# Optimization experiments

Hardware: AMD Instinct MI355X
Metric: run time of the kernel (lower is better)

## Reference

```python
import jax, jax.numpy as jnp
import numpy as np

B, C, H, W = 16, 512, 32, 32
MID = max(8, C // 4)      # gate hidden
CA_MID = max(8, C // 4)   # channel-attn hidden
LOW_RADIUS = 0.35


def dct_mat(N):
    # Orthonormal DCT-II matrix: D[k,n] = s_k * sqrt(2/N) * cos(pi*(2n+1)*k/(2N))
    k = jnp.arange(N, dtype=jnp.float32)[:, None]
    n = jnp.arange(N, dtype=jnp.float32)[None, :]
    M = jnp.cos(jnp.pi * (2.0 * n + 1.0) * k / (2.0 * N)) * jnp.sqrt(2.0 / N)
    return M.at[0].multiply(1.0 / jnp.sqrt(2.0))


def build_low_mask(Hh, Ww, low_radius):
    yy = jnp.arange(Hh, dtype=jnp.float32)[:, None] / max(Hh - 1, 1)
    xx = jnp.arange(Ww, dtype=jnp.float32)[None, :] / max(Ww - 1, 1)
    rr = jnp.sqrt(yy ** 2 + xx ** 2)
    rr = rr / jnp.maximum(rr.max(), 1e-6)
    return (rr <= low_radius).astype(jnp.float32)[None, None]  # [1,1,H,W]


def conv1x1(x, w, b):
    # x: [B,Cin,H,W], w: [Cout,Cin], b: [Cout]
    return jnp.einsum('bchw,oc->bohw', x, w) + b[None, :, None, None]


def freq_transform(x, gw1, gb1, gw2, gb2, Dh, Dw, lm):
    # gate: avgpool -> 1x1 -> relu -> 1x1 -> sigmoid, output 2 scalars per sample
    pooled = jnp.mean(x, axis=(2, 3), keepdims=True)  # [B,C,1,1]
    g = jax.nn.sigmoid(conv1x1(jax.nn.relu(conv1x1(pooled, gw1, gb1)), gw2, gb2))
    g_low, g_high = g[:, 0:1], g[:, 1:2]  # [B,1,1,1]
    # 2D ortho DCT: Dh @ x @ Dw^T
    freq = jnp.einsum('ih,bchw->bciw', Dh, x)
    freq = jnp.einsum('jw,bchw->bchj', Dw, freq)
    # frequency gating fused
    gated = freq * (g_low * lm + g_high * (1.0 - lm))
    # inverse: Dh^T @ freq @ Dw
    out = jnp.einsum('hi,bchw->bciw', Dh, gated)
    out = jnp.einsum('wj,bchw->bchj', Dw, out)
    return out


def setup_inputs() -> dict:
    key = jax.random.key(0)
    ks = jax.random.split(key, 24)
    s = 1.0 / np.sqrt(C)
    d = {
        'rgb': jax.random.normal(ks[0], (B, C, H, W), jnp.float32),
        'dsm': jax.random.normal(ks[1], (B, C, H, W), jnp.float32),
        'rgb_w': jax.random.normal(ks[2], (C, C), jnp.float32) * s,
        'rgb_b': jax.random.normal(ks[3], (C,), jnp.float32) * 0.01,
        'dsm_w': jax.random.normal(ks[4], (C, C), jnp.float32) * s,
        'dsm_b': jax.random.normal(ks[5], (C,), jnp.float32) * 0.01,
        'gate_w1': jax.random.normal(ks[6], (MID, C), jnp.float32) * s,
        'gate_b1': jax.random.normal(ks[7], (MID,), jnp.float32) * 0.01,
        'gate_w2': jax.random.normal(ks[8], (2, MID), jnp.float32) * (1.0 / np.sqrt(MID)),
        'gate_b2': jax.random.normal(ks[9], (2,), jnp.float32) * 0.01,
        'q_w': jax.random.normal(ks[10], (C, C), jnp.float32) * s,
        'q_b': jax.random.normal(ks[11], (C,), jnp.float32) * 0.01,
        'k_w': jax.random.normal(ks[12], (C, C), jnp.float32) * s,
        'k_b': jax.random.normal(ks[13], (C,), jnp.float32) * 0.01,
        'v_w': jax.random.normal(ks[14], (C, C), jnp.float32) * s,
        'v_b': jax.random.normal(ks[15], (C,), jnp.float32) * 0.01,
        'sp_w': jax.random.normal(ks[16], (C, C, 3, 3), jnp.float32) * (s / 3.0),
        'sp_b': jax.random.normal(ks[17], (C,), jnp.float32) * 0.01,
        'ca_w1': jax.random.normal(ks[18], (CA_MID, C), jnp.float32) * s,
        'ca_b1': jax.random.normal(ks[19], (CA_MID,), jnp.float32) * 0.01,
        'ca_w2': jax.random.normal(ks[20], (C, CA_MID), jnp.float32) * (1.0 / np.sqrt(CA_MID)),
        'ca_b2': jax.random.normal(ks[21], (C,), jnp.float32) * 0.01,
    }
    return d


def reference(rgb, dsm, rgb_w, rgb_b, dsm_w, dsm_b, gate_w1, gate_b1, gate_w2, gate_b2,
              q_w, q_b, k_w, k_b, v_w, v_b, sp_w, sp_b, ca_w1, ca_b1, ca_w2, ca_b2):
    Dh, Dw = dct_mat(H), dct_mat(W)
    lm = build_low_mask(H, W, LOW_RADIUS)

    rgb_p = conv1x1(rgb, rgb_w, rgb_b)
    dsm_p = conv1x1(dsm, dsm_w, dsm_b)

    rgb_f = freq_transform(rgb_p, gate_w1, gate_b1, gate_w2, gate_b2, Dh, Dw, lm)
    dsm_f = freq_transform(dsm_p, gate_w1, gate_b1, gate_w2, gate_b2, Dh, Dw, lm)

    q = conv1x1(rgb_f, q_w, q_b).reshape(B, C, H * W)
    k = conv1x1(dsm_f, k_w, k_b).reshape(B, C, H * W)
    v = conv1x1(dsm_f, v_w, v_b).reshape(B, C, H * W)

    # attn over spatial tokens: [B,N,N]
    scores = jnp.einsum('bcn,bcm->bnm', q, k) / jnp.sqrt(jnp.float32(C))
    attn = jax.nn.softmax(scores, axis=-1)
    out = jnp.einsum('bnm,bcm->bcn', attn, v).reshape(B, C, H, W)

    spatial = jax.lax.conv_general_dilated(
        out, sp_w, window_strides=(1, 1), padding='SAME',
        dimension_numbers=('NCHW', 'OIHW', 'NCHW')) + sp_b[None, :, None, None]

    pooled = jnp.mean(spatial, axis=(2, 3), keepdims=True)
    weight = jax.nn.sigmoid(conv1x1(jax.nn.relu(conv1x1(pooled, ca_w1, ca_b1)), ca_w2, ca_b2))
    return rgb_p + spatial * weight
```

## Files before the change

### kernel.cpp

```cpp
#include <hip/hip_runtime.h>

typedef long long i64;
typedef unsigned int u32;
typedef unsigned short u16;

#define Bq 16
#define Cq 512
#define Hq 32
#define Wq 32
#define Nq 1024
#define MIDq 128
#define XPBq 591872

typedef __attribute__((ext_vector_type(8))) short bf16x8;
typedef __attribute__((ext_vector_type(4))) float f32x4;

static __device__ __forceinline__ u16 f2bf(float f) {
  u32 u = __float_as_uint(f);
  u = (u + 0x7FFFu + ((u >> 16) & 1u)) >> 16;
  return (u16)u;
}
static __device__ __forceinline__ float bf2f(u16 h) {
  return __uint_as_float(((u32)h) << 16);
}

__global__ void k_dct_mask(float* __restrict__ D, float* __restrict__ lm) {
  int t = threadIdx.x;
  int i = t >> 5, j = t & 31;
  float v = cosf(3.14159265358979323846f * (2.0f * j + 1.0f) * (float)i / 64.0f) * 0.25f;
  if (i == 0) v *= 0.7071067811865476f;
  D[t] = v;
  float yy = i * (1.0f / 31.0f), xx = j * (1.0f / 31.0f);
  float rr = sqrtf(yy * yy + xx * xx) * 0.7071067811865476f;
  lm[t] = (rr <= 0.35f) ? 1.0f : 0.0f;
}

__global__ __launch_bounds__(256) void k_split(
    const float* __restrict__ src, u16* __restrict__ hi, u16* __restrict__ lo) {
  i64 idx = ((i64)blockIdx.x * 256 + threadIdx.x) * 4;
  float4 f = *(const float4*)(src + idx);
  ushort4 h, l;
  h.x = f2bf(f.x); l.x = f2bf(f.x - bf2f(h.x));
  h.y = f2bf(f.y); l.y = f2bf(f.y - bf2f(h.y));
  h.z = f2bf(f.z); l.z = f2bf(f.z - bf2f(h.z));
  h.w = f2bf(f.w); l.w = f2bf(f.w - bf2f(h.w));
  *(ushort4*)(hi + idx) = h;
  *(ushort4*)(lo + idx) = l;
}

__global__ __launch_bounds__(256) void k_zero(u16* __restrict__ p) {
  i64 idx = ((i64)blockIdx.x * 256 + threadIdx.x) * 8;
  *(uint4*)(p + idx) = (uint4){0u, 0u, 0u, 0u};
}

__global__ __launch_bounds__(256) void k_wsplit9(
    const float* __restrict__ w, u16* __restrict__ h9, u16* __restrict__ l9) {
  int idx = blockIdx.x * 256 + threadIdx.x;
  int o = idx >> 7;
  int c4 = (idx & 127) << 2;
  float vals[4][9];
#pragma unroll
  for (int j = 0; j < 4; j++) {
    const float* wp = w + ((i64)o * Cq + c4 + j) * 9;
#pragma unroll
    for (int t = 0; t < 9; t++) vals[j][t] = wp[t];
  }
#pragma unroll
  for (int t = 0; t < 9; t++) {
    ushort4 h, l;
    h.x = f2bf(vals[0][t]); l.x = f2bf(vals[0][t] - bf2f(h.x));
    h.y = f2bf(vals[1][t]); l.y = f2bf(vals[1][t] - bf2f(h.y));
    h.z = f2bf(vals[2][t]); l.z = f2bf(vals[2][t] - bf2f(h.z));
    h.w = f2bf(vals[3][t]); l.w = f2bf(vals[3][t] - bf2f(h.w));
    i64 od = (i64)t * (Cq * Cq) + (i64)o * Cq + c4;
    *(ushort4*)(h9 + od) = h;
    *(ushort4*)(l9 + od) = l;
  }
}

__global__ __launch_bounds__(256) void k_split_t(
    const float* __restrict__ src, u16* __restrict__ hi, u16* __restrict__ lo) {
  __shared__ float ld[64][65];
  int b = blockIdx.z;
  int c0 = blockIdx.y << 6;
  int n0 = blockIdx.x << 6;
  int tid = threadIdx.x;
  const float* s = src + (i64)b * (Cq * Nq);
  u16* ph = hi + (i64)b * (Cq * Nq);
  u16* pl = lo + (i64)b * (Cq * Nq);
#pragma unroll
  for (int p = 0; p < 4; p++) {
    int row = (tid >> 4) + p * 16;
    int col4 = (tid & 15) << 2;
    *(float4*)&ld[row][col4] = *(const float4*)(s + (i64)(c0 + row) * Nq + n0 + col4);
  }
  __syncthreads();
#pragma unroll
  for (int p = 0; p < 4; p++) {
    int nr = (tid >> 4) + p * 16;
    int c4 = (tid & 15) << 2;
    float f0 = ld[c4 + 0][nr], f1 = ld[c4 + 1][nr];
    float f2 = ld[c4 + 2][nr], f3 = ld[c4 + 3][nr];
    ushort4 h, l;
    h.x = f2bf(f0); l.x = f2bf(f0 - bf2f(h.x));
    h.y = f2bf(f1); l.y = f2bf(f1 - bf2f(h.y));
    h.z = f2bf(f2); l.z = f2bf(f2 - bf2f(h.z));
    h.w = f2bf(f3); l.w = f2bf(f3 - bf2f(h.w));
    i64 o = (i64)(n0 + nr) * Cq + c0 + c4;
    *(ushort4*)(ph + o) = h;
    *(ushort4*)(pl + o) = l;
  }
}

__global__ __launch_bounds__(256) void k_padsplit_t(
    const float* __restrict__ src, u16* __restrict__ hi, u16* __restrict__ lo) {
  __shared__ float ld[64][65];
  int b = blockIdx.z;
  int c0 = blockIdx.y << 6;
  int n0 = blockIdx.x << 6;
  int tid = threadIdx.x;
  const float* s = src + (i64)b * (Cq * Nq);
  u16* ph = hi + (i64)b * XPBq;
  u16* pl = lo + (i64)b * XPBq;
#pragma unroll
  for (int p = 0; p < 4; p++) {
    int row = (tid >> 4) + p * 16;
    int col4 = (tid & 15) << 2;
    *(float4*)&ld[row][col4] = *(const float4*)(s + (i64)(c0 + row) * Nq + n0 + col4);
  }
  __syncthreads();
#pragma unroll
  for (int p = 0; p < 4; p++) {
    int nr = (tid >> 4) + p * 16;
    int c4 = (tid & 15) << 2;
    float f0 = ld[c4 + 0][nr], f1 = ld[c4 + 1][nr];
    float f2 = ld[c4 + 2][nr], f3 = ld[c4 + 3][nr];
    ushort4 h, l;
    h.x = f2bf(f0); l.x = f2bf(f0 - bf2f(h.x));
    h.y = f2bf(f1); l.y = f2bf(f1 - bf2f(h.y));
    h.z = f2bf(f2); l.z = f2bf(f2 - bf2f(h.z));
    h.w = f2bf(f3); l.w = f2bf(f3 - bf2f(h.w));
    int n = n0 + nr;
    int pr = ((n >> 5) + 1) * 34 + (n & 31) + 1;
    i64 o = (i64)pr * Cq + c0 + c4;
    *(ushort4*)(ph + o) = h;
    *(ushort4*)(pl + o) = l;
  }
}

__global__ __launch_bounds__(256) void k_gemm(
    const u16* __restrict__ Ahi, const u16* __restrict__ Alo, i64 sAb,
    const u16* __restrict__ Bhi, const u16* __restrict__ Blo, i64 sBb,
    const float* __restrict__ bias, int bias_mode, float scale,
    int M, int N, int K,
    float* __restrict__ Cf, u16* __restrict__ Chi, u16* __restrict__ Clo,
    i64 sCb, int out_mode) {
  __shared__ __align__(16) u16 As_h[128][40];
  __shared__ __align__(16) u16 As_l[128][40];
  __shared__ __align__(16) u16 Bs_h[128][40];
  __shared__ __align__(16) u16 Bs_l[128][40];
  int tid = threadIdx.x;
  int b = blockIdx.z;
  int m0 = blockIdx.y << 7;
  int n0 = blockIdx.x << 7;
  const u16* pAhi = Ahi + (i64)b * sAb;
  const u16* pAlo = Alo + (i64)b * sAb;
  const u16* pBhi = Bhi + (i64)b * sBb;
  const u16* pBlo = Blo + (i64)b * sBb;
  int lane = tid & 63;
  int wid = tid >> 6;
  int wm = (wid & 1) << 6;
  int wn = (wid >> 1) << 6;
  int l15 = lane & 15;
  int g8 = (lane >> 4) << 3;
  f32x4 acc[4][4];
#pragma unroll
  for (int mi = 0; mi < 4; mi++)
#pragma unroll
    for (int nj = 0; nj < 4; nj++)
      acc[mi][nj] = (f32x4){0.f, 0.f, 0.f, 0.f};

  for (int k0 = 0; k0 < K; k0 += 32) {
#pragma unroll
    for (int i = 0; i < 8; i++) {
      const int arr = i >> 1;
      const int r = ((i & 1) << 6) + (tid >> 2);
      const int seg = tid & 3;
      uint4 val;
      if (arr == 0)      val = *(const uint4*)(pAhi + (i64)(m0 + r) * K + k0 + seg * 8);
      else if (arr == 1) val = *(const uint4*)(pAlo + (i64)(m0 + r) * K + k0 + seg * 8);
      else if (arr == 2) val = *(const uint4*)(pBhi + (i64)(n0 + r) * K + k0 + seg * 8);
      else               val = *(const uint4*)(pBlo + (i64)(n0 + r) * K + k0 + seg * 8);
      if (arr == 0)      *(uint4*)&As_h[r][seg * 8] = val;
      else if (arr == 1) *(uint4*)&As_l[r][seg * 8] = val;
      else if (arr == 2) *(uint4*)&Bs_h[r][seg * 8] = val;
      else               *(uint4*)&Bs_l[r][seg * 8] = val;
    }
    __syncthreads();
    bf16x8 ah[4], al[4], bh[4], bl[4];
#pragma unroll
    for (int mi = 0; mi < 4; mi++) {
      int row = wm + mi * 16 + l15;
      ah[mi] = *(const bf16x8*)&As_h[row][g8];
      al[mi] = *(const bf16x8*)&As_l[row][g8];
    }
#pragma unroll
    for (int nj = 0; nj < 4; nj++) {
      int row = wn + nj * 16 + l15;
      bh[nj] = *(const bf16x8*)&Bs_h[row][g8];
      bl[nj] = *(const bf16x8*)&Bs_l[row][g8];
    }
#pragma unroll
    for (int mi = 0; mi < 4; mi++)
#pragma unroll
      for (int nj = 0; nj < 4; nj++) {
        acc[mi][nj] = __builtin_amdgcn_mfma_f32_16x16x32_bf16(ah[mi], bh[nj], acc[mi][nj], 0, 0, 0);
        acc[mi][nj] = __builtin_amdgcn_mfma_f32_16x16x32_bf16(ah[mi], bl[nj], acc[mi][nj], 0, 0, 0);
        acc[mi][nj] = __builtin_amdgcn_mfma_f32_16x16x32_bf16(al[mi], bh[nj], acc[mi][nj], 0, 0, 0);
      }
    __syncthreads();
  }

#pragma unroll
  for (int mi = 0; mi < 4; mi++)
#pragma unroll
    for (int nj = 0; nj < 4; nj++) {
      int col_g = n0 + wn + nj * 16 + l15;
#pragma unroll
      for (int r = 0; r < 4; r++) {
        int row_g = m0 + wm + mi * 16 + ((lane >> 4) << 2) + r;
        float val = acc[mi][nj][r] * scale;
        if (bias_mode == 1) val += bias[row_g];
        else if (bias_mode == 2) val += bias[col_g];
        i64 o = (i64)b * sCb + (i64)row_g * N + col_g;
        if (out_mode == 0) {
          Cf[o] = val;
        } else {
          u16 h = f2bf(val);
          Chi[o] = h;
          Clo[o] = f2bf(val - bf2f(h));
        }
      }
    }
}

__global__ __launch_bounds__(256) void k_conv3_mfma(
    const u16* __restrict__ Wh, const u16* __restrict__ Wl,
    const u16* __restrict__ Xh, const u16* __restrict__ Xl,
    const float* __restrict__ bias, float* __restrict__ out) {
  __shared__ __align__(16) u16 As_h[128][40];
  __shared__ __align__(16) u16 As_l[128][40];
  __shared__ __align__(16) u16 Bs_h[128][40];
  __shared__ __align__(16) u16 Bs_l[128][40];
  int tid = threadIdx.x;
  int b = blockIdx.z;
  int m0 = blockIdx.y << 7;
  int n0 = blockIdx.x << 7;
  const u16* pXh = Xh + (i64)b * XPBq;
  const u16* pXl = Xl + (i64)b * XPBq;
  int lane = tid & 63;
  int wid = tid >> 6;
  int wm = (wid & 1) << 6;
  int wn = (wid >> 1) << 6;
  int l15 = lane & 15;
  int g8 = (lane >> 4) << 3;
  int rr = tid >> 2, seg = tid & 3;
  int n_a = n0 + rr, n_b = n0 + 64 + rr;
  int prb0 = (n_a >> 5) * 34 + (n_a & 31);
  int prb1 = (n_b >> 5) * 34 + (n_b & 31);
  f32x4 acc[4][4];
#pragma unroll
  for (int mi = 0; mi < 4; mi++)
#pragma unroll
    for (int nj = 0; nj < 4; nj++)
      acc[mi][nj] = (f32x4){0.f, 0.f, 0.f, 0.f};

  for (int tap = 0; tap < 9; tap++) {
    int doff = (tap / 3) * 34 + (tap % 3);
    const u16* wth = Wh + (i64)tap * (Cq * Cq);
    const u16* wtl = Wl + (i64)tap * (Cq * Cq);
    i64 bb0 = (i64)(prb0 + doff) * Cq + seg * 8;
    i64 bb1 = (i64)(prb1 + doff) * Cq + seg * 8;
    for (int c0 = 0; c0 < Cq; c0 += 32) {
      *(uint4*)&As_h[rr][seg * 8]      = *(const uint4*)(wth + (i64)(m0 + rr) * Cq + c0 + seg * 8);
      *(uint4*)&As_h[64 + rr][seg * 8] = *(const uint4*)(wth + (i64)(m0 + 64 + rr) * Cq + c0 + seg * 8);
      *(uint4*)&As_l[rr][seg * 8]      = *(const uint4*)(wtl + (i64)(m0 + rr) * Cq + c0 + seg * 8);
      *(uint4*)&As_l[64 + rr][seg * 8] = *(const uint4*)(wtl + (i64)(m0 + 64 + rr) * Cq + c0 + seg * 8);
      *(uint4*)&Bs_h[rr][seg * 8]      = *(const uint4*)(pXh + bb0 + c0);
      *(uint4*)&Bs_h[64 + rr][seg * 8] = *(const uint4*)(pXh + bb1 + c0);
      *(uint4*)&Bs_l[rr][seg * 8]      = *(const uint4*)(pXl + bb0 + c0);
      *(uint4*)&Bs_l[64 + rr][seg * 8] = *(const uint4*)(pXl + bb1 + c0);
      __syncthreads();
      bf16x8 ah[4], al[4], bh[4], bl[4];
#pragma unroll
      for (int mi = 0; mi < 4; mi++) {
        int row = wm + mi * 16 + l15;
        ah[mi] = *(const bf16x8*)&As_h[row][g8];
        al[mi] = *(const bf16x8*)&As_l[row][g8];
      }
#pragma unroll
      for (int nj = 0; nj < 4; nj++) {
        int row = wn + nj * 16 + l15;
        bh[nj] = *(const bf16x8*)&Bs_h[row][g8];
        bl[nj] = *(const bf16x8*)&Bs_l[row][g8];
      }
#pragma unroll
      for (int mi = 0; mi < 4; mi++)
#pragma unroll
        for (int nj = 0; nj < 4; nj++) {
          acc[mi][nj] = __builtin_amdgcn_mfma_f32_16x16x32_bf16(ah[mi], bh[nj], acc[mi][nj], 0, 0, 0);
          acc[mi][nj] = __builtin_amdgcn_mfma_f32_16x16x32_bf16(ah[mi], bl[nj], acc[mi][nj], 0, 0, 0);
          acc[mi][nj] = __builtin_amdgcn_mfma_f32_16x16x32_bf16(al[mi], bh[nj], acc[mi][nj], 0, 0, 0);
        }
      __syncthreads();
    }
  }

#pragma unroll
  for (int mi = 0; mi < 4; mi++)
#pragma unroll
    for (int nj = 0; nj < 4; nj++) {
      int col_g = n0 + wn + nj * 16 + l15;
#pragma unroll
      for (int r = 0; r < 4; r++) {
        int row_g = m0 + wm + mi * 16 + ((lane >> 4) << 2) + r;
        float val = acc[mi][nj][r] + bias[row_g];
        out[(i64)b * (Cq * Nq) + (i64)row_g * Nq + col_g] = val;
      }
    }
}

__global__ __launch_bounds__(256) void k_pool(const float* __restrict__ x, float* __restrict__ o) {
  int gw = (int)((blockIdx.x * 256 + threadIdx.x) >> 6);
  int ln = threadIdx.x & 63;
  const float* p = x + (i64)gw * Nq;
  float s = 0.f;
#pragma unroll
  for (int it = 0; it < 4; it++) {
    float4 v = *(const float4*)(p + ln * 4 + it * 256);
    s += v.x + v.y + v.z + v.w;
  }
#pragma unroll
  for (int off = 32; off > 0; off >>= 1) s += __shfl_xor(s, off, 64);
  if (ln == 0) o[gw] = s * (1.0f / 1024.0f);
}

__global__ __launch_bounds__(128) void k_gate(
    const float* __restrict__ pooled, const float* __restrict__ w1,
    const float* __restrict__ b1, const float* __restrict__ w2,
    const float* __restrict__ b2, float* __restrict__ g) {
  __shared__ float pl[Cq];
  __shared__ float h[MIDq];
  int b = blockIdx.x, tid = threadIdx.x;
  for (int c = tid; c < Cq; c += 128) pl[c] = pooled[b * Cq + c];
  __syncthreads();
  float s = b1[tid];
  const float* wr = w1 + (i64)tid * Cq;
  for (int c = 0; c < Cq; c++) s = fmaf(wr[c], pl[c], s);
  h[tid] = fmaxf(s, 0.f);
  __syncthreads();
  if (tid < 2) {
    float t = b2[tid];
    const float* w2r = w2 + tid * MIDq;
    for (int m = 0; m < MIDq; m++) t = fmaf(w2r[m], h[m], t);
    g[b * 2 + tid] = 1.0f / (1.0f + expf(-t));
  }
}

__global__ __launch_bounds__(256) void k_freq(
    const float* __restrict__ xr, const float* __restrict__ xd,
    float* __restrict__ yr, float* __restrict__ yd,
    const float* __restrict__ g_r, const float* __restrict__ g_d,
    const float* __restrict__ Dm, const float* __restrict__ lm) {
  __shared__ float Ds[32][36], Dt[32][36], Xs[32][36], T1[32][36];
  int bid = blockIdx.x;
  const float* x; float* y; const float* g;
  if (bid < Bq * Cq) {
    x = xr + (i64)bid * Nq; y = yr + (i64)bid * Nq; g = g_r + (bid >> 9) * 2;
  } else {
    int id = bid - Bq * Cq;
    x = xd + (i64)id * Nq; y = yd + (i64)id * Nq; g = g_d + (id >> 9) * 2;
  }
  int tid = threadIdx.x;
  int r_ = tid >> 3, j4 = (tid & 7) << 2;
  {
    float4 dv = *(const float4*)(Dm + tid * 4);
    *(float4*)&Ds[r_][j4] = dv;
    Dt[j4 + 0][r_] = dv.x; Dt[j4 + 1][r_] = dv.y;
    Dt[j4 + 2][r_] = dv.z; Dt[j4 + 3][r_] = dv.w;
    *(float4*)&Xs[r_][j4] = *(const float4*)(x + tid * 4);
  }
  float gl = g[0], gh = g[1];
  __syncthreads();
  float a0 = 0, a1 = 0, a2 = 0, a3 = 0;
#pragma unroll
  for (int h = 0; h < 32; h++) {
    float a = Ds[r_][h];
    float4 bv = *(const float4*)&Xs[h][j4];
    a0 = fmaf(a, bv.x, a0); a1 = fmaf(a, bv.y, a1);
    a2 = fmaf(a, bv.z, a2); a3 = fmaf(a, bv.w, a3);
  }
  *(float4*)&T1[r_][j4] = make_float4(a0, a1, a2, a3);
  __syncthreads();
  a0 = a1 = a2 = a3 = 0;
#pragma unroll
  for (int w = 0; w < 32; w++) {
    float a = T1[r_][w];
    float4 bv = *(const float4*)&Dt[w][j4];
    a0 = fmaf(a, bv.x, a0); a1 = fmaf(a, bv.y, a1);
    a2 = fmaf(a, bv.z, a2); a3 = fmaf(a, bv.w, a3);
  }
  {
    float4 mv = *(const float4*)(lm + r_ * 32 + j4);
    a0 *= fmaf(gl, mv.x, gh * (1.f - mv.x));
    a1 *= fmaf(gl, mv.y, gh * (1.f - mv.y));
    a2 *= fmaf(gl, mv.z, gh * (1.f - mv.z));
    a3 *= fmaf(gl, mv.w, gh * (1.f - mv.w));
  }
  __syncthreads();
  *(float4*)&Xs[r_][j4] = make_float4(a0, a1, a2, a3);
  __syncthreads();
  a0 = a1 = a2 = a3 = 0;
#pragma unroll
  for (int ii = 0; ii < 32; ii++) {
    float a = Dt[r_][ii];
    float4 bv = *(const float4*)&Xs[ii][j4];
    a0 = fmaf(a, bv.x, a0); a1 = fmaf(a, bv.y, a1);
    a2 = fmaf(a, bv.z, a2); a3 = fmaf(a, bv.w, a3);
  }
  __syncthreads();
  *(float4*)&T1[r_][j4] = make_float4(a0, a1, a2, a3);
  __syncthreads();
  a0 = a1 = a2 = a3 = 0;
#pragma unroll
  for (int jj = 0; jj < 32; jj++) {
    float a = T1[r_][jj];
    float4 bv = *(const float4*)&Ds[jj][j4];
    a0 = fmaf(a, bv.x, a0); a1 = fmaf(a, bv.y, a1);
    a2 = fmaf(a, bv.z, a2); a3 = fmaf(a, bv.w, a3);
  }
  *(float4*)(y + tid * 4) = make_float4(a0, a1, a2, a3);
}

__global__ __launch_bounds__(256) void k_softmax_split(
    const float* __restrict__ sc, u16* __restrict__ ahi, u16* __restrict__ alo) {
  __shared__ float redm[4], reds[4];
  i64 row = blockIdx.x;
  const float* p = sc + row * (i64)Nq;
  int tid = threadIdx.x;
  float4 v = ((const float4*)p)[tid];
  float mx = fmaxf(fmaxf(v.x, v.y), fmaxf(v.z, v.w));
#pragma unroll
  for (int o = 32; o > 0; o >>= 1) mx = fmaxf(mx, __shfl_xor(mx, o, 64));
  if ((tid & 63) == 0) redm[tid >> 6] = mx;
  __syncthreads();
  mx = fmaxf(fmaxf(redm[0], redm[1]), fmaxf(redm[2], redm[3]));
  v.x = expf(v.x - mx); v.y = expf(v.y - mx);
  v.z = expf(v.z - mx); v.w = expf(v.w - mx);
  float s = v.x + v.y + v.z + v.w;
#pragma unroll
  for (int o = 32; o > 0; o >>= 1) s += __shfl_xor(s, o, 64);
  if ((tid & 63) == 0) reds[tid >> 6] = s;
  __syncthreads();
  s = reds[0] + reds[1] + reds[2] + reds[3];
  float inv = 1.0f / s;
  v.x *= inv; v.y *= inv; v.z *= inv; v.w *= inv;
  ushort4 h, l;
  h.x = f2bf(v.x); l.x = f2bf(v.x - bf2f(h.x));
  h.y = f2bf(v.y); l.y = f2bf(v.y - bf2f(h.y));
  h.z = f2bf(v.z); l.z = f2bf(v.z - bf2f(h.z));
  h.w = f2bf(v.w); l.w = f2bf(v.w - bf2f(h.w));
  *(ushort4*)(ahi + row * Nq + tid * 4) = h;
  *(ushort4*)(alo + row * Nq + tid * 4) = l;
}

__global__ __launch_bounds__(512) void k_ca(
    const float* __restrict__ pooled, const float* __restrict__ w1,
    const float* __restrict__ b1, const float* __restrict__ w2,
    const float* __restrict__ b2, float* __restrict__ wt) {
  __shared__ float pl[Cq];
  __shared__ float h[MIDq];
  int b = blockIdx.x, tid = threadIdx.x;
  pl[tid] = pooled[b * Cq + tid];
  __syncthreads();
  if (tid < MIDq) {
    float s = b1[tid];
    const float* wr = w1 + (i64)tid * Cq;
    for (int c = 0; c < Cq; c++) s = fmaf(wr[c], pl[c], s);
    h[tid] = fmaxf(s, 0.f);
  }
  __syncthreads();
  float s = b2[tid];
  const float* wr = w2 + (i64)tid * MIDq;
  for (int m = 0; m < MIDq; m++) s = fmaf(wr[m], h[m], s);
  wt[b * Cq + tid] = 1.0f / (1.0f + expf(-s));
}

__global__ __launch_bounds__(256) void k_final(
    const float* __restrict__ rgbp, const float* __restrict__ sp,
    const float* __restrict__ wt, float* __restrict__ out) {
  i64 idx = (i64)blockIdx.x * 256 + threadIdx.x;
  float4 a = ((const float4*)rgbp)[idx];
  float4 s = ((const float4*)sp)[idx];
  float w = wt[idx >> 8];
  float4 r;
  r.x = fmaf(s.x, w, a.x); r.y = fmaf(s.y, w, a.y);
  r.z = fmaf(s.z, w, a.z); r.w = fmaf(s.w, w, a.w);
  ((float4*)out)[idx] = r;
}

extern "C" void kernel_launch(void* const* d_in, const int* in_sizes, int n_in,
                              void* d_out, int out_size, void* d_ws, size_t ws_size,
                              hipStream_t stream) {
  (void)in_sizes; (void)n_in; (void)out_size; (void)ws_size;
  const float* rgb    = (const float*)d_in[0];
  const float* dsm    = (const float*)d_in[1];
  const float* rgb_w  = (const float*)d_in[2];
  const float* rgb_b  = (const float*)d_in[3];
  const float* dsm_w  = (const float*)d_in[4];
  const float* dsm_b  = (const float*)d_in[5];
  const float* gate_w1 = (const float*)d_in[6];
  const float* gate_b1 = (const float*)d_in[7];
  const float* gate_w2 = (const float*)d_in[8];
  const float* gate_b2 = (const float*)d_in[9];
  const float* q_w = (const float*)d_in[10];
  const float* q_b = (const float*)d_in[11];
  const float* k_w = (const float*)d_in[12];
  const float* k_b = (const float*)d_in[13];
  const float* v_w = (const float*)d_in[14];
  const float* v_b = (const float*)d_in[15];
  const float* sp_w = (const float*)d_in[16];
  const float* sp_b = (const float*)d_in[17];
  const float* ca_w1 = (const float*)d_in[18];
  const float* ca_b1 = (const float*)d_in[19];
  const float* ca_w2 = (const float*)d_in[20];
  const float* ca_b2 = (const float*)d_in[21];

  const i64 S  = (i64)Bq * Cq * Nq;
  const i64 SU = S;
  const i64 WE = (i64)Cq * Cq;
  const i64 XPT = (i64)Bq * XPBq;

  float* wsf = (float*)d_ws;
  float* rgbp   = wsf;
  float* dsmp   = wsf + S;
  float* rgbf   = wsf + 2 * S;
  float* dsmf   = wsf + 3 * S;
  float* scores  = dsmp;
  float* attout  = dsmf;
  float* spatial = dsmp;
  float* smallr = wsf + 4 * S;
  float* Dm     = smallr;
  float* lm     = smallr + 1024;
  float* pooled = smallr + 2048;
  float* g_rgb  = smallr + 10240;
  float* g_dsm  = smallr + 10272;
  float* wt     = smallr + 10304;
  u16* ub = (u16*)(wsf + 4 * S + 32768);
  u16* U0 = ub;          u16* U1 = ub + SU;
  u16* U2 = ub + 2 * SU; u16* U3 = ub + 3 * SU;
  u16* U4 = ub + 4 * SU; u16* U5 = ub + 5 * SU;
  u16* XPh = ub;
  u16* XPl = ub + XPT;
  u16* wb = ub + 6 * SU;
  u16* rgbw_h = wb;           u16* rgbw_l = wb + WE;
  u16* dsmw_h = wb + 2 * WE;  u16* dsmw_l = wb + 3 * WE;
  u16* qw_h   = wb + 4 * WE;  u16* qw_l   = wb + 5 * WE;
  u16* kw_h   = wb + 6 * WE;  u16* kw_l   = wb + 7 * WE;
  u16* vw_h   = wb + 8 * WE;  u16* vw_l   = wb + 9 * WE;
  u16* w9h    = wb + 10 * WE; u16* w9l    = wb + 19 * WE;

  const i64 sT = (i64)Nq * Cq;
  const i64 sS = (i64)Nq * Nq;
  const float rsqc = 0.044194173824159216f;

  k_dct_mask<<<1, 1024, 0, stream>>>(Dm, lm);

  k_split<<<WE / 1024, 256, 0, stream>>>(rgb_w, rgbw_h, rgbw_l);
  k_split<<<WE / 1024, 256, 0, stream>>>(dsm_w, dsmw_h, dsmw_l);
  k_split<<<WE / 1024, 256, 0, stream>>>(q_w, qw_h, qw_l);
  k_split<<<WE / 1024, 256, 0, stream>>>(k_w, kw_h, kw_l);
  k_split<<<WE / 1024, 256, 0, stream>>>(v_w, vw_h, vw_l);
  k_wsplit9<<<256, 256, 0, stream>>>(sp_w, w9h, w9l);

  dim3 gT(Nq / 64, Cq / 64, Bq);
  dim3 gW(Nq / 128, Cq / 128, Bq);
  dim3 gQ(Cq / 128, Nq / 128, Bq);
  dim3 gS(Nq / 128, Nq / 128, Bq);

  k_split_t<<<gT, 256, 0, stream>>>(rgb, U0, U1);
  k_gemm<<<gW, 256, 0, stream>>>(rgbw_h, rgbw_l, 0, U0, U1, sT,
                                 rgb_b, 1, 1.0f, Cq, Nq, Cq,
                                 rgbp, nullptr, nullptr, sT, 0);
  k_split_t<<<gT, 256, 0, stream>>>(dsm, U0, U1);
  k_gemm<<<gW, 256, 0, stream>>>(dsmw_h, dsmw_l, 0, U0, U1, sT,
                                 dsm_b, 1, 1.0f, Cq, Nq, Cq,
                                 dsmp, nullptr, nullptr, sT, 0);

  k_pool<<<(Bq * Cq) / 4, 256, 0, stream>>>(rgbp, pooled);
  k_gate<<<Bq, 128, 0, stream>>>(pooled, gate_w1, gate_b1, gate_w2, gate_b2, g_rgb);
  k_pool<<<(Bq * Cq) / 4, 256, 0, stream>>>(dsmp, pooled);
  k_gate<<<Bq, 128, 0, stream>>>(pooled, gate_w1, gate_b1, gate_w2, gate_b2, g_dsm);

  k_freq<<<2 * Bq * Cq, 256, 0, stream>>>(rgbp, dsmp, rgbf, dsmf, g_rgb, g_dsm, Dm, lm);

  k_split_t<<<gT, 256, 0, stream>>>(rgbf, U0, U1);
  k_split_t<<<gT, 256, 0, stream>>>(dsmf, U2, U3);

  k_gemm<<<gQ, 256, 0, stream>>>(U0, U1, sT, qw_h, qw_l, 0,
                                 q_b, 2, 1.0f, Nq, Cq, Cq,
                                 nullptr, U4, U5, sT, 1);
  k_gemm<<<gQ, 256, 0, stream>>>(U2, U3, sT, kw_h, kw_l, 0,
                                 k_b, 2, 1.0f, Nq, Cq, Cq,
                                 nullptr, U0, U1, sT, 1);
  k_gemm<<<gS, 256, 0, stream>>>(U4, U5, sT, U0, U1, sT,
                                 nullptr, 0, rsqc, Nq, Nq, Cq,
                                 scores, nullptr, nullptr, sS, 0);
  k_gemm<<<gW, 256, 0, stream>>>(vw_h, vw_l, 0, U2, U3, sT,
                                 v_b, 1, 1.0f, Cq, Nq, Cq,
                                 nullptr, U4, U5, sT, 1);
  k_softmax_split<<<Bq * Nq, 256, 0, stream>>>(scores, U0, U2);
  k_gemm<<<gW, 256, 0, stream>>>(U4, U5, sT, U0, U2, sS,
                                 nullptr, 0, 1.0f, Cq, Nq, Nq,
                                 attout, nullptr, nullptr, sT, 0);

  k_zero<<<(int)(2 * XPT / 8 / 256), 256, 0, stream>>>(XPh);
  k_padsplit_t<<<gT, 256, 0, stream>>>(attout, XPh, XPl);
  k_conv3_mfma<<<dim3(Nq / 128, Cq / 128, Bq), 256, 0, stream>>>(
      w9h, w9l, XPh, XPl, sp_b, spatial);

  k_pool<<<(Bq * Cq) / 4, 256, 0, stream>>>(spatial, pooled);
  k_ca<<<Bq, 512, 0, stream>>>(pooled, ca_w1, ca_b1, ca_w2, ca_b2, wt);

  k_final<<<(int)(S / 4 / 256), 256, 0, stream>>>(rgbp, spatial, wt, (float*)d_out);
}
```

Measured before the change: 857.1 us.

## Fuse fp32 split into GEMM loads, merge prep kernels, remap workgroups across XCDs

The GEMM can now read fp32 activations directly and split them into bf16 hi/lo inside the shared-memory load, so the separate transpose-and-split passes over rgb, dsm, rgbf and dsmf go away. All weight splitting and the DCT/mask setup are merged into one prep kernel. Pool and gate run as single launches over both branches. Only the padding border is zeroed instead of the whole padded buffer. GEMM and conv workgroup indices are remapped round-robin over 8 chunks to spread them across XCDs. The in-GEMM split adds conversion ALU work and strided fp32 loads to every K tile, and the low half is now truncated rather than rounded.

```diff
diff --git a/kernel.cpp b/kernel.cpp
--- a/kernel.cpp
+++ b/kernel.cpp
@@ -24,92 +24,79 @@
   return __uint_as_float(((u32)h) << 16);
 }
 
-__global__ void k_dct_mask(float* __restrict__ D, float* __restrict__ lm) {
-  int t = threadIdx.x;
-  int i = t >> 5, j = t & 31;
-  float v = cosf(3.14159265358979323846f * (2.0f * j + 1.0f) * (float)i / 64.0f) * 0.25f;
-  if (i == 0) v *= 0.7071067811865476f;
-  D[t] = v;
-  float yy = i * (1.0f / 31.0f), xx = j * (1.0f / 31.0f);
-  float rr = sqrtf(yy * yy + xx * xx) * 0.7071067811865476f;
-  lm[t] = (rr <= 0.35f) ? 1.0f : 0.0f;
-}
-
-__global__ __launch_bounds__(256) void k_split(
-    const float* __restrict__ src, u16* __restrict__ hi, u16* __restrict__ lo) {
-  i64 idx = ((i64)blockIdx.x * 256 + threadIdx.x) * 4;
-  float4 f = *(const float4*)(src + idx);
-  ushort4 h, l;
-  h.x = f2bf(f.x); l.x = f2bf(f.x - bf2f(h.x));
-  h.y = f2bf(f.y); l.y = f2bf(f.y - bf2f(h.y));
-  h.z = f2bf(f.z); l.z = f2bf(f.z - bf2f(h.z));
-  h.w = f2bf(f.w); l.w = f2bf(f.w - bf2f(h.w));
-  *(ushort4*)(hi + idx) = h;
-  *(ushort4*)(lo + idx) = l;
-}
-
-__global__ __launch_bounds__(256) void k_zero(u16* __restrict__ p) {
-  i64 idx = ((i64)blockIdx.x * 256 + threadIdx.x) * 8;
-  *(uint4*)(p + idx) = (uint4){0u, 0u, 0u, 0u};
-}
-
-__global__ __launch_bounds__(256) void k_wsplit9(
-    const float* __restrict__ w, u16* __restrict__ h9, u16* __restrict__ l9) {
-  int idx = blockIdx.x * 256 + threadIdx.x;
-  int o = idx >> 7;
-  int c4 = (idx & 127) << 2;
-  float vals[4][9];
-#pragma unroll
-  for (int j = 0; j < 4; j++) {
-    const float* wp = w + ((i64)o * Cq + c4 + j) * 9;
-#pragma unroll
-    for (int t = 0; t < 9; t++) vals[j][t] = wp[t];
-  }
-#pragma unroll
-  for (int t = 0; t < 9; t++) {
+__global__ __launch_bounds__(256) void k_prep(
+    const float* __restrict__ rgb_w, const float* __restrict__ dsm_w,
+    const float* __restrict__ q_w, const float* __restrict__ k_w,
+    const float* __restrict__ v_w, const float* __restrict__ sp_w,
+    u16* __restrict__ rw_h, u16* __restrict__ rw_l,
+    u16* __restrict__ dw_h, u16* __restrict__ dw_l,
+    u16* __restrict__ qw_h, u16* __restrict__ qw_l,
+    u16* __restrict__ kw_h, u16* __restrict__ kw_l,
+    u16* __restrict__ vw_h, u16* __restrict__ vw_l,
+    u16* __restrict__ w9h, u16* __restrict__ w9l,
+    float* __restrict__ Dm, float* __restrict__ lm) {
+  int blk = blockIdx.x, tid = threadIdx.x;
+  if (blk < 1280) {
+    int wi = blk >> 8;
+    const float* src = wi == 0 ? rgb_w : wi == 1 ? dsm_w : wi == 2 ? q_w : wi == 3 ? k_w : v_w;
+    u16* hi = wi == 0 ? rw_h : wi == 1 ? dw_h : wi == 2 ? qw_h : wi == 3 ? kw_h : vw_h;
+    u16* lo = wi == 0 ? rw_l : wi == 1 ? dw_l : wi == 2 ? qw_l : wi == 3 ? kw_l : vw_l;
+    i64 idx = ((i64)(blk & 255) * 256 + tid) * 4;
+    float4 f = *(const float4*)(src + idx);
     ushort4 h, l;
-    h.x = f2bf(vals[0][t]); l.x = f2bf(vals[0][t] - bf2f(h.x));
-    h.y = f2bf(vals[1][t]); l.y = f2bf(vals[1][t] - bf2f(h.y));
-    h.z = f2bf(vals[2][t]); l.z = f2bf(vals[2][t] - bf2f(h.z));
-    h.w = f2bf(vals[3][t]); l.w = f2bf(vals[3][t] - bf2f(h.w));
-    i64 od = (i64)t * (Cq * Cq) + (i64)o * Cq + c4;
-    *(ushort4*)(h9 + od) = h;
-    *(ushort4*)(l9 + od) = l;
-  }
-}
-
-__global__ __launch_bounds__(256) void k_split_t(
-    const float* __restrict__ src, u16* __restrict__ hi, u16* __restrict__ lo) {
-  __shared__ float ld[64][65];
-  int b = blockIdx.z;
-  int c0 = blockIdx.y << 6;
-  int n0 = blockIdx.x << 6;
-  int tid = threadIdx.x;
-  const float* s = src + (i64)b * (Cq * Nq);
-  u16* ph = hi + (i64)b * (Cq * Nq);
-  u16* pl = lo + (i64)b * (Cq * Nq);
-#pragma unroll
-  for (int p = 0; p < 4; p++) {
-    int row = (tid >> 4) + p * 16;
-    int col4 = (tid & 15) << 2;
-    *(float4*)&ld[row][col4] = *(const float4*)(s + (i64)(c0 + row) * Nq + n0 + col4);
-  }
-  __syncthreads();
-#pragma unroll
-  for (int p = 0; p < 4; p++) {
-    int nr = (tid >> 4) + p * 16;
-    int c4 = (tid & 15) << 2;
-    float f0 = ld[c4 + 0][nr], f1 = ld[c4 + 1][nr];
-    float f2 = ld[c4 + 2][nr], f3 = ld[c4 + 3][nr];
-    ushort4 h, l;
-    h.x = f2bf(f0); l.x = f2bf(f0 - bf2f(h.x));
-    h.y = f2bf(f1); l.y = f2bf(f1 - bf2f(h.y));
-    h.z = f2bf(f2); l.z = f2bf(f2 - bf2f(h.z));
-    h.w = f2bf(f3); l.w = f2bf(f3 - bf2f(h.w));
-    i64 o = (i64)(n0 + nr) * Cq + c0 + c4;
-    *(ushort4*)(ph + o) = h;
-    *(ushort4*)(pl + o) = l;
-  }
+    h.x = f2bf(f.x); l.x = f2bf(f.x - bf2f(h.x));
+    h.y = f2bf(f.y); l.y = f2bf(f.y - bf2f(h.y));
+    h.z = f2bf(f.z); l.z = f2bf(f.z - bf2f(h.z));
+    h.w = f2bf(f.w); l.w = f2bf(f.w - bf2f(h.w));
+    *(ushort4*)(hi + idx) = h;
+    *(ushort4*)(lo + idx) = l;
+  } else if (blk < 1536) {
+    int idx = (blk - 1280) * 256 + tid;
+    int o = idx >> 7;
+    int c4 = (idx & 127) << 2;
+    float vals[4][9];
+#pragma unroll
+    for (int j = 0; j < 4; j++) {
+      const float* wp = sp_w + ((i64)o * Cq + c4 + j) * 9;
+#pragma unroll
+      for (int t = 0; t < 9; t++) vals[j][t] = wp[t];
+    }
+#pragma unroll
+    for (int t = 0; t < 9; t++) {
+      ushort4 h, l;
+      h.x = f2bf(vals[0][t]); l.x = f2bf(vals[0][t] - bf2f(h.x));
+      h.y = f2bf(vals[1][t]); l.y = f2bf(vals[1][t] - bf2f(h.y));
+      h.z = f2bf(vals[2][t]); l.z = f2bf(vals[2][t] - bf2f(h.z));
+      h.w = f2bf(vals[3][t]); l.w = f2bf(vals[3][t] - bf2f(h.w));
+      i64 od = (i64)t * (Cq * Cq) + (i64)o * Cq + c4;
+      *(ushort4*)(w9h + od) = h;
+      *(ushort4*)(w9l + od) = l;
+    }
+  } else {
+#pragma unroll
+    for (int q4 = 0; q4 < 4; q4++) {
+      int t = tid * 4 + q4;
+      int i = t >> 5, j = t & 31;
+      float v = cosf(3.14159265358979323846f * (2.0f * j + 1.0f) * (float)i / 64.0f) * 0.25f;
+      if (i == 0) v *= 0.7071067811865476f;
+      Dm[t] = v;
+      float yy = i * (1.0f / 31.0f), xx = j * (1.0f / 31.0f);
+      float rr = sqrtf(yy * yy + xx * xx) * 0.7071067811865476f;
+      lm[t] = (rr <= 0.35f) ? 1.0f : 0.0f;
+    }
+  }
+}
+
+__global__ __launch_bounds__(64) void k_zero_border(u16* __restrict__ xp) {
+  int i = blockIdx.x;
+  int b = blockIdx.y;
+  int arr = blockIdx.z;
+  int pr;
+  if (i < 34) pr = i;
+  else if (i < 68) pr = 33 * 34 + (i - 34);
+  else { int j = i - 68; pr = (1 + (j >> 1)) * 34 + (j & 1) * 33; }
+  u16* p = xp + (i64)arr * ((i64)Bq * XPBq) + (i64)b * XPBq + (i64)pr * Cq;
+  *(uint4*)(p + threadIdx.x * 8) = (uint4){0u, 0u, 0u, 0u};
 }
 
 __global__ __launch_bounds__(256) void k_padsplit_t(
@@ -149,8 +136,10 @@
 }
 
 __global__ __launch_bounds__(256) void k_gemm(
-    const u16* __restrict__ Ahi, const u16* __restrict__ Alo, i64 sAb,
-    const u16* __restrict__ Bhi, const u16* __restrict__ Blo, i64 sBb,
+    const u16* __restrict__ Ahi, const u16* __restrict__ Alo,
+    const float* __restrict__ Af32, int a_mode, i64 sAb,
+    const u16* __restrict__ Bhi, const u16* __restrict__ Blo,
+    const float* __restrict__ Bf32, int b_mode, i64 sBb,
     const float* __restrict__ bias, int bias_mode, float scale,
     int M, int N, int K,
     float* __restrict__ Cf, u16* __restrict__ Chi, u16* __restrict__ Clo,
@@ -160,13 +149,20 @@
   __shared__ __align__(16) u16 Bs_h[128][40];
   __shared__ __align__(16) u16 Bs_l[128][40];
   int tid = threadIdx.x;
-  int b = blockIdx.z;
-  int m0 = blockIdx.y << 7;
-  int n0 = blockIdx.x << 7;
-  const u16* pAhi = Ahi + (i64)b * sAb;
-  const u16* pAlo = Alo + (i64)b * sAb;
-  const u16* pBhi = Bhi + (i64)b * sBb;
-  const u16* pBlo = Blo + (i64)b * sBb;
+  int gx = gridDim.x, gxy = gx * gridDim.y;
+  int nwg = gxy * gridDim.z;
+  int orig = blockIdx.x + gx * blockIdx.y + gxy * blockIdx.z;
+  int wg = (nwg & 7) ? orig : ((orig & 7) * (nwg >> 3) + (orig >> 3));
+  int b = wg / gxy;
+  int rem = wg - b * gxy;
+  int m0 = (rem / gx) << 7;
+  int n0 = (rem - (rem / gx) * gx) << 7;
+  const u16* pAhi = Ahi + (i64)b * (a_mode ? 0 : sAb);
+  const u16* pAlo = Alo + (i64)b * (a_mode ? 0 : sAb);
+  const float* pAf = a_mode ? (Af32 + (i64)b * sAb) : nullptr;
+  const u16* pBhi = Bhi + (i64)b * (b_mode ? 0 : sBb);
+  const u16* pBlo = Blo + (i64)b * (b_mode ? 0 : sBb);
+  const float* pBf = b_mode ? (Bf32 + (i64)b * sBb) : nullptr;
   int lane = tid & 63;
   int wid = tid >> 6;
   int wm = (wid & 1) << 6;
@@ -181,20 +177,65 @@
       acc[mi][nj] = (f32x4){0.f, 0.f, 0.f, 0.f};
 
   for (int k0 = 0; k0 < K; k0 += 32) {
-#pragma unroll
-    for (int i = 0; i < 8; i++) {
-      const int arr = i >> 1;
-      const int r = ((i & 1) << 6) + (tid >> 2);
-      const int seg = tid & 3;
-      uint4 val;
-      if (arr == 0)      val = *(const uint4*)(pAhi + (i64)(m0 + r) * K + k0 + seg * 8);
-      else if (arr == 1) val = *(const uint4*)(pAlo + (i64)(m0 + r) * K + k0 + seg * 8);
-      else if (arr == 2) val = *(const uint4*)(pBhi + (i64)(n0 + r) * K + k0 + seg * 8);
-      else               val = *(const uint4*)(pBlo + (i64)(n0 + r) * K + k0 + seg * 8);
-      if (arr == 0)      *(uint4*)&As_h[r][seg * 8] = val;
-      else if (arr == 1) *(uint4*)&As_l[r][seg * 8] = val;
-      else if (arr == 2) *(uint4*)&Bs_h[r][seg * 8] = val;
-      else               *(uint4*)&Bs_l[r][seg * 8] = val;
+    if (a_mode == 0) {
+#pragma unroll
+      for (int i = 0; i < 4; i++) {
+        int r = ((i & 1) << 6) + (tid >> 2);
+        int seg = tid & 3;
+        const u16* src = (i < 2) ? pAhi : pAlo;
+        uint4 val = *(const uint4*)(src + (i64)(m0 + r) * K + k0 + seg * 8);
+        if (i < 2) *(uint4*)&As_h[r][seg * 8] = val;
+        else       *(uint4*)&As_l[r][seg * 8] = val;
+      }
+    } else {
+      int cs = tid >> 6, ns = tid & 63;
+      const float* src = pAf + (i64)(k0 + cs * 8) * M + m0 + ns * 2;
+      float2 f[8];
+#pragma unroll
+      for (int j = 0; j < 8; j++) f[j] = *(const float2*)(src + (i64)j * M);
+#pragma unroll
+      for (int i = 0; i < 2; i++) {
+        union { u16 u[8]; uint4 v; } hh, ll;
+#pragma unroll
+        for (int j = 0; j < 8; j++) {
+          float x = i ? f[j].y : f[j].x;
+          u16 h = f2bf(x);
+          hh.u[j] = h;
+          ll.u[j] = (u16)(__float_as_uint(x - bf2f(h)) >> 16);
+        }
+        *(uint4*)&As_h[2 * ns + i][8 * cs] = hh.v;
+        *(uint4*)&As_l[2 * ns + i][8 * cs] = ll.v;
+      }
+    }
+    if (b_mode == 0) {
+#pragma unroll
+      for (int i = 0; i < 4; i++) {
+        int r = ((i & 1) << 6) + (tid >> 2);
+        int seg = tid & 3;
+        const u16* src = (i < 2) ? pBhi : pBlo;
+        uint4 val = *(const uint4*)(src + (i64)(n0 + r) * K + k0 + seg * 8);
+        if (i < 2) *(uint4*)&Bs_h[r][seg * 8] = val;
+        else       *(uint4*)&Bs_l[r][seg * 8] = val;
+      }
+    } else {
+      int cs = tid >> 6, ns = tid & 63;
+      const float* src = pBf + (i64)(k0 + cs * 8) * N + n0 + ns * 2;
+      float2 f[8];
+#pragma unroll
+      for (int j = 0; j < 8; j++) f[j] = *(const float2*)(src + (i64)j * N);
+#pragma unroll
+      for (int i = 0; i < 2; i++) {
+        union { u16 u[8]; uint4 v; } hh, ll;
+#pragma unroll
+        for (int j = 0; j < 8; j++) {
+          float x = i ? f[j].y : f[j].x;
+          u16 h = f2bf(x);
+          hh.u[j] = h;
+          ll.u[j] = (u16)(__float_as_uint(x - bf2f(h)) >> 16);
+        }
+        *(uint4*)&Bs_h[2 * ns + i][8 * cs] = hh.v;
+        *(uint4*)&Bs_l[2 * ns + i][8 * cs] = ll.v;
+      }
     }
     __syncthreads();
     bf16x8 ah[4], al[4], bh[4], bl[4];
@@ -253,9 +294,14 @@
   __shared__ __align__(16) u16 Bs_h[128][40];
   __shared__ __align__(16) u16 Bs_l[128][40];
   int tid = threadIdx.x;
-  int b = blockIdx.z;
-  int m0 = blockIdx.y << 7;
-  int n0 = blockIdx.x << 7;
+  int gx = gridDim.x, gxy = gx * gridDim.y;
+  int nwg = gxy * gridDim.z;
+  int orig = blockIdx.x + gx * blockIdx.y + gxy * blockIdx.z;
+  int wg = (nwg & 7) ? orig : ((orig & 7) * (nwg >> 3) + (orig >> 3));
+  int b = wg / gxy;
+  int rem = wg - b * gxy;
+  int m0 = (rem / gx) << 7;
+  int n0 = (rem - (rem / gx) * gx) << 7;
   const u16* pXh = Xh + (i64)b * XPBq;
   const u16* pXl = Xl + (i64)b * XPBq;
   int lane = tid & 63;
@@ -351,8 +397,8 @@
     const float* __restrict__ b2, float* __restrict__ g) {
   __shared__ float pl[Cq];
   __shared__ float h[MIDq];
-  int b = blockIdx.x, tid = threadIdx.x;
-  for (int c = tid; c < Cq; c += 128) pl[c] = pooled[b * Cq + c];
+  int bb = blockIdx.x, tid = threadIdx.x;
+  for (int c = tid; c < Cq; c += 128) pl[c] = pooled[bb * Cq + c];
   __syncthreads();
   float s = b1[tid];
   const float* wr = w1 + (i64)tid * Cq;
@@ -363,7 +409,7 @@
     float t = b2[tid];
     const float* w2r = w2 + tid * MIDq;
     for (int m = 0; m < MIDq; m++) t = fmaf(w2r[m], h[m], t);
-    g[b * 2 + tid] = 1.0f / (1.0f + expf(-t));
+    g[bb * 2 + tid] = 1.0f / (1.0f + expf(-t));
   }
 }
 
@@ -553,13 +599,13 @@
   float* Dm     = smallr;
   float* lm     = smallr + 1024;
   float* pooled = smallr + 2048;
-  float* g_rgb  = smallr + 10240;
-  float* g_dsm  = smallr + 10272;
-  float* wt     = smallr + 10304;
+  float* g_all  = smallr + 18432;
+  float* wt     = smallr + 18496;
   u16* ub = (u16*)(wsf + 4 * S + 32768);
   u16* U0 = ub;          u16* U1 = ub + SU;
   u16* U2 = ub + 2 * SU; u16* U3 = ub + 3 * SU;
   u16* U4 = ub + 4 * SU; u16* U5 = ub + 5 * SU;
+  (void)U1; (void)U3; (void)U5;
   u16* XPh = ub;
   u16* XPl = ub + XPT;
   u16* wb = ub + 6 * SU;
@@ -574,58 +620,52 @@
   const i64 sS = (i64)Nq * Nq;
   const float rsqc = 0.044194173824159216f;
 
-  k_dct_mask<<<1, 1024, 0, stream>>>(Dm, lm);
-
-  k_split<<<WE / 1024, 256, 0, stream>>>(rgb_w, rgbw_h, rgbw_l);
-  k_split<<<WE / 1024, 256, 0, stream>>>(dsm_w, dsmw_h, dsmw_l);
-  k_split<<<WE / 1024, 256, 0, stream>>>(q_w, qw_h, qw_l);
-  k_split<<<WE / 1024, 256, 0, stream>>>(k_w, kw_h, kw_l);
-  k_split<<<WE / 1024, 256, 0, stream>>>(v_w, vw_h, vw_l);
-  k_wsplit9<<<256, 256, 0, stream>>>(sp_w, w9h, w9l);
-
-  dim3 gT(Nq / 64, Cq / 64, Bq);
+  k_prep<<<1537, 256, 0, stream>>>(rgb_w, dsm_w, q_w, k_w, v_w, sp_w,
+                                   rgbw_h, rgbw_l, dsmw_h, dsmw_l, qw_h, qw_l,
+                                   kw_h, kw_l, vw_h, vw_l, w9h, w9l, Dm, lm);
+
   dim3 gW(Nq / 128, Cq / 128, Bq);
   dim3 gQ(Cq / 128, Nq / 128, Bq);
   dim3 gS(Nq / 128, Nq / 128, Bq);
 
-  k_split_t<<<gT, 256, 0, stream>>>(rgb, U0, U1);
-  k_gemm<<<gW, 256, 0, stream>>>(rgbw_h, rgbw_l, 0, U0, U1, sT,
+  k_gemm<<<gW, 256, 0, stream>>>(rgbw_h, rgbw_l, nullptr, 0, 0,
+                                 nullptr, nullptr, rgb, 1, sT,
                                  rgb_b, 1, 1.0f, Cq, Nq, Cq,
                                  rgbp, nullptr, nullptr, sT, 0);
-  k_split_t<<<gT, 256, 0, stream>>>(dsm, U0, U1);
-  k_gemm<<<gW, 256, 0, stream>>>(dsmw_h, dsmw_l, 0, U0, U1, sT,
+  k_gemm<<<gW, 256, 0, stream>>>(dsmw_h, dsmw_l, nullptr, 0, 0,
+                                 nullptr, nullptr, dsm, 1, sT,
                                  dsm_b, 1, 1.0f, Cq, Nq, Cq,
                                  dsmp, nullptr, nullptr, sT, 0);
 
-  k_pool<<<(Bq * Cq) / 4, 256, 0, stream>>>(rgbp, pooled);
-  k_gate<<<Bq, 128, 0, stream>>>(pooled, gate_w1, gate_b1, gate_w2, gate_b2, g_rgb);
-  k_pool<<<(Bq * Cq) / 4, 256, 0, stream>>>(dsmp, pooled);
-  k_gate<<<Bq, 128, 0, stream>>>(pooled, gate_w1, gate_b1, gate_w2, gate_b2, g_dsm);
-
-  k_freq<<<2 * Bq * Cq, 256, 0, stream>>>(rgbp, dsmp, rgbf, dsmf, g_rgb, g_dsm, Dm, lm);
-
-  k_split_t<<<gT, 256, 0, stream>>>(rgbf, U0, U1);
-  k_split_t<<<gT, 256, 0, stream>>>(dsmf, U2, U3);
-
-  k_gemm<<<gQ, 256, 0, stream>>>(U0, U1, sT, qw_h, qw_l, 0,
+  k_pool<<<(2 * Bq * Cq) / 4, 256, 0, stream>>>(rgbp, pooled);
+  k_gate<<<32, 128, 0, stream>>>(pooled, gate_w1, gate_b1, gate_w2, gate_b2, g_all);
+
+  k_freq<<<2 * Bq * Cq, 256, 0, stream>>>(rgbp, dsmp, rgbf, dsmf, g_all, g_all + 32, Dm, lm);
+
+  k_gemm<<<gQ, 256, 0, stream>>>(nullptr, nullptr, rgbf, 1, sT,
+                                 qw_h, qw_l, nullptr, 0, 0,
                                  q_b, 2, 1.0f, Nq, Cq, Cq,
                                  nullptr, U4, U5, sT, 1);
-  k_gemm<<<gQ, 256, 0, stream>>>(U2, U3, sT, kw_h, kw_l, 0,
+  k_gemm<<<gQ, 256, 0, stream>>>(nullptr, nullptr, dsmf, 1, sT,
+                                 kw_h, kw_l, nullptr, 0, 0,
                                  k_b, 2, 1.0f, Nq, Cq, Cq,
                                  nullptr, U0, U1, sT, 1);
-  k_gemm<<<gS, 256, 0, stream>>>(U4, U5, sT, U0, U1, sT,
+  k_gemm<<<gS, 256, 0, stream>>>(U4, U5, nullptr, 0, sT,
+                                 U0, U1, nullptr, 0, sT,
                                  nullptr, 0, rsqc, Nq, Nq, Cq,
                                  scores, nullptr, nullptr, sS, 0);
-  k_gemm<<<gW, 256, 0, stream>>>(vw_h, vw_l, 0, U2, U3, sT,
+  k_gemm<<<gW, 256, 0, stream>>>(vw_h, vw_l, nullptr, 0, 0,
+                                 nullptr, nullptr, dsmf, 1, sT,
                                  v_b, 1, 1.0f, Cq, Nq, Cq,
                                  nullptr, U4, U5, sT, 1);
   k_softmax_split<<<Bq * Nq, 256, 0, stream>>>(scores, U0, U2);
-  k_gemm<<<gW, 256, 0, stream>>>(U4, U5, sT, U0, U2, sS,
+  k_gemm<<<gW, 256, 0, stream>>>(U4, U5, nullptr, 0, sT,
+                                 U0, U2, nullptr, 0, sS,
                                  nullptr, 0, 1.0f, Cq, Nq, Nq,
                                  attout, nullptr, nullptr, sT, 0);
 
-  k_zero<<<(int)(2 * XPT / 8 / 256), 256, 0, stream>>>(XPh);
-  k_padsplit_t<<<gT, 256, 0, stream>>>(attout, XPh, XPl);
+  k_zero_border<<<dim3(132, Bq, 2), 64, 0, stream>>>(XPh);
+  k_padsplit_t<<<dim3(Nq / 64, Cq / 64, Bq), 256, 0, stream>>>(attout, XPh, XPl);
   k_conv3_mfma<<<dim3(Nq / 128, Cq / 128, Bq), 256, 0, stream>>>(
       w9h, w9l, XPh, XPl, sp_b, spatial);
 
```

New measurement: 783.9 us. 8.5% less time.
